# Kernel optimization log

Hardware: AMD Instinct MI355X
Metric: run time of the kernel (lower is better)

Reference implementation:

```python
import jax, jax.numpy as jnp
import numpy as np

DIM, D_INNER, D_STATE, D_CONV, DT_RANK = 768, 1536, 16, 4, 48
B, L = 2, 1024

def setup_inputs() -> dict:
    key = jax.random.key(0)
    ks = jax.random.split(key, 10)
    s = lambda fan: 1.0 / np.sqrt(fan)
    return {
        'x': jax.random.normal(ks[0], (B, L, DIM), jnp.float32),
        'ln_w': jnp.ones((DIM,), jnp.float32),
        'ln_b': jnp.zeros((DIM,), jnp.float32),
        'in_proj_w': jax.random.normal(ks[1], (2 * D_INNER, DIM), jnp.float32) * s(DIM),
        'conv_w': jax.random.normal(ks[2], (D_INNER, D_CONV), jnp.float32) * s(D_CONV),
        'conv_b': jnp.zeros((D_INNER,), jnp.float32),
        'x_proj_w': jax.random.normal(ks[3], (DT_RANK + 2 * D_STATE, D_INNER), jnp.float32) * s(D_INNER),
        'dt_proj_w': jax.random.normal(ks[4], (D_INNER, DT_RANK), jnp.float32) * s(DT_RANK),
        'dt_proj_b': jax.random.normal(ks[5], (D_INNER,), jnp.float32) * 0.1 - 4.0,  # softplus ~ small dt
        'A_log': jnp.log(jnp.broadcast_to(jnp.arange(1, D_STATE + 1, dtype=jnp.float32), (D_INNER, D_STATE))),
        'D_param': jnp.ones((D_INNER,), jnp.float32),
        'out_proj_w': jax.random.normal(ks[6], (DIM, D_INNER), jnp.float32) * s(D_INNER),
    }

def _silu(v):
    return v * jax.nn.sigmoid(v)

def reference(x, ln_w, ln_b, in_proj_w, conv_w, conv_b, x_proj_w,
              dt_proj_w, dt_proj_b, A_log, D_param, out_proj_w):
    Bb, Ll, _ = x.shape
    # LayerNorm (eps=1e-5, torch default)
    mu = jnp.mean(x, -1, keepdims=True)
    var = jnp.mean(jnp.square(x - mu), -1, keepdims=True)
    xn = (x - mu) * jax.lax.rsqrt(var + 1e-5) * ln_w + ln_b
    # in_proj -> (B,L,2*d_inner), split into x-branch and gate z
    xz = xn @ in_proj_w.T
    xm, z = jnp.split(xz, 2, axis=-1)
    # causal depthwise conv1d, kernel D_CONV, left-pad D_CONV-1
    xp = jnp.pad(xm, ((0, 0), (D_CONV - 1, 0), (0, 0)))
    xc = conv_b + sum(xp[:, k:k + Ll, :] * conv_w[:, k] for k in range(D_CONV))
    u = _silu(xc)  # (B,L,d_inner)
    # input-dependent dt, B, C
    dbc = u @ x_proj_w.T
    dt, Bm, Cm = jnp.split(dbc, [DT_RANK, DT_RANK + D_STATE], axis=-1)
    delta = jax.nn.softplus(dt @ dt_proj_w.T + dt_proj_b)  # (B,L,d_inner)
    A = -jnp.exp(A_log)  # (d_inner, d_state), negative
    dA = jnp.exp(delta[..., None] * A)                      # (B,L,D,N)
    dBu = (delta * u)[..., None] * Bm[:, :, None, :]        # (B,L,D,N)
    # linear recurrence h_t = dA_t * h_{t-1} + dBu_t via associative scan
    def comb(e1, e2):
        a1, b1 = e1
        a2, b2 = e2
        return a1 * a2, a2 * b1 + b2
    _, h = jax.lax.associative_scan(comb, (dA, dBu), axis=1)
    y = jnp.einsum('bldn,bln->bld', h, Cm) + u * D_param
    y = y * _silu(z)
    return y @ out_proj_w.T
```

## Files before the change

### kernel.cpp

```cpp
#include <hip/hip_runtime.h>
#include <hip/hip_bf16.h>

#define BATCH 2
#define SEQ   1024
#define DIM   768
#define DI    1536
#define DS    16
#define DCONV 4
#define DTR   48
#define XZW   (2*DI)
#define DBCW  (DTR+2*DS)
#define MROWS (BATCH*SEQ)
#define NCHUNK 32
#define CLEN  (SEQ/NCHUNK)
#define XP_KS 8
#define OP_KS 4

typedef unsigned short ushort_t;
typedef __attribute__((ext_vector_type(8))) short short8;
typedef __attribute__((ext_vector_type(4))) float f32x4;

__device__ __forceinline__ float sigmoidf_(float x) {
    return 1.f / (1.f + __expf(-x));
}

__device__ __forceinline__ ushort_t f2bf(float x) {
    union { float f; unsigned u; } c{x};
    unsigned r = c.u + 0x7FFF + ((c.u >> 16) & 1);
    return (ushort_t)(r >> 16);
}

__device__ __forceinline__ void gload16(const void* g, void* lds) {
    __builtin_amdgcn_global_load_lds(
        (const __attribute__((address_space(1))) void*)g,
        (__attribute__((address_space(3))) void*)lds,
        16, 0, 0);
}

__global__ __launch_bounds__(256) void cvt_bf16(const float* __restrict__ in,
                                                ushort_t* __restrict__ out, int n)
{
    int i = (blockIdx.x * 256 + threadIdx.x) * 8;
    if (i >= n) return;
    float4 a = *(const float4*)(in + i);
    float4 b = *(const float4*)(in + i + 4);
    ushort_t o[8] = { f2bf(a.x), f2bf(a.y), f2bf(a.z), f2bf(a.w),
                      f2bf(b.x), f2bf(b.y), f2bf(b.z), f2bf(b.w) };
    *(ushort4*)(out + i)     = *(ushort4*)o;
    *(ushort4*)(out + i + 4) = *(ushort4*)(o + 4);
}

__global__ __launch_bounds__(256) void at_kernel(const float* __restrict__ A_log,
                                                 float* __restrict__ aT)
{
    int i = blockIdx.x * 256 + threadIdx.x;
    if (i >= DS * DI) return;
    int n = i / DI, d = i % DI;
    aT[i] = -__expf(A_log[d * DS + n]) * 1.44269504f;
}

__global__ __launch_bounds__(256) void reduce_sk4(const float4* __restrict__ part,
                                                  float4* __restrict__ out,
                                                  int count4, int nslices)
{
    int i = blockIdx.x * 256 + threadIdx.x;
    if (i >= count4) return;
    float4 s = part[i];
    for (int z = 1; z < nslices; ++z) {
        float4 p = part[(size_t)z * count4 + i];
        s.x += p.x; s.y += p.y; s.z += p.z; s.w += p.w;
    }
    out[i] = s;
}

__global__ __launch_bounds__(256) void ln_kernel(const float* __restrict__ x,
                                                 const float* __restrict__ w,
                                                 const float* __restrict__ b,
                                                 ushort_t* __restrict__ xn)
{
    __shared__ float part[8];
    int row = blockIdx.x;
    const float* xr = x + (size_t)row * DIM;
    ushort_t* o = xn + (size_t)row * DIM;
    int tid = threadIdx.x;
    int lane = tid & 63, wid = tid >> 6;

    float v0 = xr[tid], v1 = xr[tid + 256], v2 = xr[tid + 512];
    float s = v0 + v1 + v2;
    #pragma unroll
    for (int off = 32; off > 0; off >>= 1) s += __shfl_xor(s, off);
    if (lane == 0) part[wid] = s;
    __syncthreads();
    float mu = (part[0] + part[1] + part[2] + part[3]) * (1.f / DIM);

    float d0 = v0 - mu, d1 = v1 - mu, d2 = v2 - mu;
    float q = d0 * d0 + d1 * d1 + d2 * d2;
    #pragma unroll
    for (int off = 32; off > 0; off >>= 1) q += __shfl_xor(q, off);
    if (lane == 0) part[4 + wid] = q;
    __syncthreads();
    float rstd = rsqrtf((part[4] + part[5] + part[6] + part[7]) * (1.f / DIM) + 1e-5f);

    o[tid]       = f2bf(d0 * rstd * w[tid]       + b[tid]);
    o[tid + 256] = f2bf(d1 * rstd * w[tid + 256] + b[tid + 256]);
    o[tid + 512] = f2bf(d2 * rstd * w[tid + 512] + b[tid + 512]);
}

__global__ __launch_bounds__(256) void gemm_bf16(const ushort_t* __restrict__ A,
                                                 const ushort_t* __restrict__ W,
                                                 float* __restrict__ C,
                                                 int N, int K)
{
    __shared__ __align__(16) ushort_t As[128 * 32];
    __shared__ __align__(16) ushort_t Bs[128 * 32];

    int tid = threadIdx.x;
    int wave = tid >> 6, lane = tid & 63;
    int wr = wave >> 1, wc = wave & 1;
    int l15 = lane & 15, kb = lane >> 4;
    int m0 = blockIdx.y * 128, n0 = blockIdx.x * 128;

    f32x4 acc[4][4] = {};

    for (int k0 = 0; k0 < K; k0 += 32) {
        #pragma unroll
        for (int i = 0; i < 2; ++i) {
            int cbase = i * 256 + wave * 64;
            int c = cbase + lane;
            int row = c >> 2;
            int col = (c & 3) * 8;
            gload16(A + (size_t)(m0 + row) * K + k0 + col, (char*)As + (size_t)cbase * 16);
            gload16(W + (size_t)(n0 + row) * K + k0 + col, (char*)Bs + (size_t)cbase * 16);
        }
        __syncthreads();

        short8 af[4], bfr[4];
        #pragma unroll
        for (int m = 0; m < 4; ++m)
            af[m] = *(const short8*)&As[(wr * 64 + m * 16 + l15) * 32 + kb * 8];
        #pragma unroll
        for (int n = 0; n < 4; ++n)
            bfr[n] = *(const short8*)&Bs[(wc * 64 + n * 16 + l15) * 32 + kb * 8];

        #pragma unroll
        for (int m = 0; m < 4; ++m)
            #pragma unroll
            for (int n = 0; n < 4; ++n)
                acc[m][n] = __builtin_amdgcn_mfma_f32_16x16x32_bf16(af[m], bfr[n], acc[m][n], 0, 0, 0);

        __syncthreads();
    }

    int r0 = m0 + wr * 64 + kb * 4;
    int c0 = n0 + wc * 64 + l15;
    #pragma unroll
    for (int m = 0; m < 4; ++m)
        #pragma unroll
        for (int n = 0; n < 4; ++n) {
            int rr = r0 + m * 16;
            int cc = c0 + n * 16;
            #pragma unroll
            for (int r = 0; r < 4; ++r)
                C[(size_t)(rr + r) * N + cc] = acc[m][n][r];
        }
}

__global__ __launch_bounds__(256) void gemm_bf16_sk(const ushort_t* __restrict__ A,
                                                    const ushort_t* __restrict__ W,
                                                    float* __restrict__ Cpart,
                                                    int N, int Ktot, int Kslice, int M)
{
    __shared__ __align__(16) ushort_t As[128 * 32];
    __shared__ __align__(16) ushort_t Bs[128 * 32];

    int tid = threadIdx.x;
    int wave = tid >> 6, lane = tid & 63;
    int wr = wave >> 1, wc = wave & 1;
    int l15 = lane & 15, kb = lane >> 4;
    int m0 = blockIdx.y * 128, n0 = blockIdx.x * 128;
    int kbase = blockIdx.z * Kslice;
    float* C = Cpart + (size_t)blockIdx.z * M * N;

    f32x4 acc[4][4] = {};

    for (int k0 = kbase; k0 < kbase + Kslice; k0 += 32) {
        #pragma unroll
        for (int i = 0; i < 2; ++i) {
            int cbase = i * 256 + wave * 64;
            int c = cbase + lane;
            int row = c >> 2;
            int col = (c & 3) * 8;
            gload16(A + (size_t)(m0 + row) * Ktot + k0 + col, (char*)As + (size_t)cbase * 16);
            gload16(W + (size_t)(n0 + row) * Ktot + k0 + col, (char*)Bs + (size_t)cbase * 16);
        }
        __syncthreads();

        short8 af[4], bfr[4];
        #pragma unroll
        for (int m = 0; m < 4; ++m)
            af[m] = *(const short8*)&As[(wr * 64 + m * 16 + l15) * 32 + kb * 8];
        #pragma unroll
        for (int n = 0; n < 4; ++n)
            bfr[n] = *(const short8*)&Bs[(wc * 64 + n * 16 + l15) * 32 + kb * 8];

        #pragma unroll
        for (int m = 0; m < 4; ++m)
            #pragma unroll
            for (int n = 0; n < 4; ++n)
                acc[m][n] = __builtin_amdgcn_mfma_f32_16x16x32_bf16(af[m], bfr[n], acc[m][n], 0, 0, 0);

        __syncthreads();
    }

    int r0 = m0 + wr * 64 + kb * 4;
    int c0 = n0 + wc * 64 + l15;
    #pragma unroll
    for (int m = 0; m < 4; ++m)
        #pragma unroll
        for (int n = 0; n < 4; ++n) {
            int rr = r0 + m * 16;
            int cc = c0 + n * 16;
            #pragma unroll
            for (int r = 0; r < 4; ++r)
                C[(size_t)(rr + r) * N + cc] = acc[m][n][r];
        }
}

__global__ __launch_bounds__(256) void gemm_nt(const float* __restrict__ A, int lda,
                                               const float* __restrict__ W, int ldw,
                                               float* __restrict__ C, int ldc,
                                               int N, int K,
                                               const float* __restrict__ bias, int act)
{
    __shared__ float As[64][17];
    __shared__ float Ws[64][17];
    int tid = threadIdx.x;
    int tx = tid & 15;
    int ty = tid >> 4;
    int m0 = blockIdx.y * 64;
    int n0 = blockIdx.x * 64;

    float acc[4][4] = {};

    for (int k0 = 0; k0 < K; k0 += 16) {
        #pragma unroll
        for (int i = 0; i < 4; ++i) {
            int idx = tid + i * 256;
            int r = idx >> 4, c = idx & 15;
            As[r][c] = A[(size_t)(m0 + r) * lda + k0 + c];
            int nr = n0 + r;
            Ws[r][c] = (nr < N) ? W[(size_t)nr * ldw + k0 + c] : 0.f;
        }
        __syncthreads();
        #pragma unroll
        for (int kk = 0; kk < 16; ++kk) {
            float av[4], wv[4];
            #pragma unroll
            for (int i = 0; i < 4; ++i) av[i] = As[ty * 4 + i][kk];
            #pragma unroll
            for (int j = 0; j < 4; ++j) wv[j] = Ws[tx * 4 + j][kk];
            #pragma unroll
            for (int i = 0; i < 4; ++i)
                #pragma unroll
                for (int j = 0; j < 4; ++j)
                    acc[i][j] += av[i] * wv[j];
        }
        __syncthreads();
    }

    #pragma unroll
    for (int i = 0; i < 4; ++i) {
        int m = m0 + ty * 4 + i;
        #pragma unroll
        for (int j = 0; j < 4; ++j) {
            int n = n0 + tx * 4 + j;
            if (n < N) {
                float v = acc[i][j];
                if (bias) v += bias[n];
                if (act == 1) v = (v > 20.f) ? v : log1pf(__expf(v));
                C[(size_t)m * ldc + n] = v;
            }
        }
    }
}

__global__ __launch_bounds__(256) void gemm_nt_sk(const float* __restrict__ A, int lda,
                                                  const float* __restrict__ W, int ldw,
                                                  float* __restrict__ Cpart, int ldc,
                                                  int N, int Kslice, int M)
{
    __shared__ float As[64][17];
    __shared__ float Ws[64][17];
    int tid = threadIdx.x;
    int tx = tid & 15;
    int ty = tid >> 4;
    int m0 = blockIdx.y * 64;
    int n0 = blockIdx.x * 64;
    int kbase = blockIdx.z * Kslice;
    float* C = Cpart + (size_t)blockIdx.z * M * ldc;

    float acc[4][4] = {};

    for (int k0 = kbase; k0 < kbase + Kslice; k0 += 16) {
        #pragma unroll
        for (int i = 0; i < 4; ++i) {
            int idx = tid + i * 256;
            int r = idx >> 4, c = idx & 15;
            As[r][c] = A[(size_t)(m0 + r) * lda + k0 + c];
            int nr = n0 + r;
            Ws[r][c] = (nr < N) ? W[(size_t)nr * ldw + k0 + c] : 0.f;
        }
        __syncthreads();
        #pragma unroll
        for (int kk = 0; kk < 16; ++kk) {
            float av[4], wv[4];
            #pragma unroll
            for (int i = 0; i < 4; ++i) av[i] = As[ty * 4 + i][kk];
            #pragma unroll
            for (int j = 0; j < 4; ++j) wv[j] = Ws[tx * 4 + j][kk];
            #pragma unroll
            for (int i = 0; i < 4; ++i)
                #pragma unroll
                for (int j = 0; j < 4; ++j)
                    acc[i][j] += av[i] * wv[j];
        }
        __syncthreads();
    }

    #pragma unroll
    for (int i = 0; i < 4; ++i) {
        int m = m0 + ty * 4 + i;
        #pragma unroll
        for (int j = 0; j < 4; ++j) {
            int n = n0 + tx * 4 + j;
            if (n < N)
                C[(size_t)m * ldc + n] = acc[i][j];
        }
    }
}

__global__ __launch_bounds__(256) void conv_silu_kernel(const float* __restrict__ xz,
                                                        const float* __restrict__ cw,
                                                        const float* __restrict__ cb,
                                                        float* __restrict__ u)
{
    int idx = blockIdx.x * 256 + threadIdx.x;
    int d4 = idx % (DI / 4);
    int bt = idx / (DI / 4);
    int t = bt % SEQ;
    int b = bt / SEQ;
    int d = d4 * 4;

    float4 w0 = *(const float4*)(cw + (d + 0) * 4);
    float4 w1 = *(const float4*)(cw + (d + 1) * 4);
    float4 w2 = *(const float4*)(cw + (d + 2) * 4);
    float4 w3 = *(const float4*)(cw + (d + 3) * 4);
    const float* wp[4] = { (const float*)&w0, (const float*)&w1,
                           (const float*)&w2, (const float*)&w3 };

    float4 acc = *(const float4*)(cb + d);
    #pragma unroll
    for (int k = 0; k < DCONV; ++k) {
        int tt = t - (DCONV - 1) + k;
        if (tt >= 0) {
            float4 xv = *(const float4*)(xz + (size_t)(b * SEQ + tt) * XZW + d);
            acc.x += xv.x * wp[0][k];
            acc.y += xv.y * wp[1][k];
            acc.z += xv.z * wp[2][k];
            acc.w += xv.w * wp[3][k];
        }
    }
    acc.x *= sigmoidf_(acc.x);
    acc.y *= sigmoidf_(acc.y);
    acc.z *= sigmoidf_(acc.z);
    acc.w *= sigmoidf_(acc.w);
    *(float4*)(u + (size_t)(b * SEQ + t) * DI + d) = acc;
}


__global__ __launch_bounds__(256) void scan_p1(const float* __restrict__ delta,
                                               const float* __restrict__ u,
                                               const float* __restrict__ dbc,
                                               const float* __restrict__ aT,
                                               float* __restrict__ Pw,
                                               float* __restrict__ Sw)
{
    __shared__ float Bs[4][CLEN][DS];
    int tid = threadIdx.x;
    int lane = tid & 63, w = tid >> 6;
    int d = blockIdx.x * 64 + lane;
    int chunk = blockIdx.y * 4 + w;
    int b = blockIdx.z;
    int t0 = chunk * CLEN;

    #pragma unroll
    for (int i = 0; i < 2; ++i) {
        int idx = i * 64 + lane;
        int tl = idx >> 2, c = idx & 3;
        *(float4*)&Bs[w][tl][c * 4] =
            *(const float4*)(dbc + (size_t)(b * SEQ + t0 + tl) * DBCW + DTR + c * 4);
    }

    float a[DS];
    #pragma unroll
    for (int n = 0; n < DS; ++n) a[n] = aT[n * DI + d];

    __syncthreads();

    float P[DS], S[DS];
    #pragma unroll
    for (int n = 0; n < DS; ++n) { P[n] = 1.f; S[n] = 0.f; }

    const float* dp = delta + ((size_t)b * SEQ + t0) * DI + d;
    const float* up = u     + ((size_t)b * SEQ + t0) * DI + d;
    #pragma unroll 4
    for (int j = 0; j < CLEN; ++j) {
        float dlt = dp[(size_t)j * DI];
        float uu  = up[(size_t)j * DI];
        float dltu = dlt * uu;
        #pragma unroll
        for (int n = 0; n < DS; ++n) {
            float dA = exp2f(dlt * a[n]);
            P[n] *= dA;
            S[n] = dA * S[n] + dltu * Bs[w][j][n];
        }
    }

    size_t base = (((size_t)b * NCHUNK + chunk) * DS) * DI + d;
    #pragma unroll
    for (int n = 0; n < DS; ++n) {
        Pw[base + (size_t)n * DI] = P[n];
        Sw[base + (size_t)n * DI] = S[n];
    }
}

__global__ __launch_bounds__(256) void scan_comb(const float* __restrict__ Pw,
                                                 const float* __restrict__ Sw,
                                                 float* __restrict__ Hin)
{
    int d = blockIdx.x * 256 + threadIdx.x;
    int n = blockIdx.y, b = blockIdx.z;
    float h = 0.f;
    for (int c = 0; c < NCHUNK; ++c) {
        size_t idx = (((size_t)b * NCHUNK + c) * DS + n) * DI + d;
        Hin[idx] = h;
        h = Pw[idx] * h + Sw[idx];
    }
}

__global__ __launch_bounds__(256) void scan_p3(const float* __restrict__ delta,
                                               const float* __restrict__ u,
                                               const float* __restrict__ dbc,
                                               const float* __restrict__ xz,
                                               const float* __restrict__ aT,
                                               const float* __restrict__ Dp,
                                               const float* __restrict__ Hin,
                                               ushort_t* __restrict__ y)
{
    __shared__ float Bs[4][CLEN][2 * DS];
    int tid = threadIdx.x;
    int lane = tid & 63, w = tid >> 6;
    int d = blockIdx.x * 64 + lane;
    int chunk = blockIdx.y * 4 + w;
    int b = blockIdx.z;
    int t0 = chunk * CLEN;

    #pragma unroll
    for (int i = 0; i < 4; ++i) {
        int idx = i * 64 + lane;
        int tl = idx >> 3, c = idx & 7;
        *(float4*)&Bs[w][tl][c * 4] =
            *(const float4*)(dbc + (size_t)(b * SEQ + t0 + tl) * DBCW + DTR + c * 4);
    }

    float a[DS], h[DS];
    #pragma unroll
    for (int n = 0; n < DS; ++n) a[n] = aT[n * DI + d];
    size_t hbase = (((size_t)b * NCHUNK + chunk) * DS) * DI + d;
    #pragma unroll
    for (int n = 0; n < DS; ++n) h[n] = Hin[hbase + (size_t)n * DI];

    float Dd = Dp[d];
    __syncthreads();

    const float* dp = delta + ((size_t)b * SEQ + t0) * DI + d;
    const float* up = u     + ((size_t)b * SEQ + t0) * DI + d;
    const float* zp = xz    + ((size_t)b * SEQ + t0) * XZW + DI + d;
    ushort_t* yp    = y     + ((size_t)b * SEQ + t0) * DI + d;

    #pragma unroll 2
    for (int j = 0; j < CLEN; ++j) {
        float dlt = dp[(size_t)j * DI];
        float uu  = up[(size_t)j * DI];
        float dltu = dlt * uu;
        #pragma unroll
        for (int n = 0; n < DS; ++n) {
            float dA = exp2f(dlt * a[n]);
            h[n] = dA * h[n] + dltu * Bs[w][j][n];
        }
        float p0 = 0.f, p1 = 0.f, p2 = 0.f, p3 = 0.f;
        #pragma unroll
        for (int n = 0; n < DS; n += 4) {
            p0 += h[n]     * Bs[w][j][DS + n];
            p1 += h[n + 1] * Bs[w][j][DS + n + 1];
            p2 += h[n + 2] * Bs[w][j][DS + n + 2];
            p3 += h[n + 3] * Bs[w][j][DS + n + 3];
        }
        float p = (p0 + p1) + (p2 + p3);
        float z = zp[(size_t)j * XZW];
        float yv = (p + uu * Dd) * (z * sigmoidf_(z));
        yp[(size_t)j * DI] = f2bf(yv);
    }
}

extern "C" void kernel_launch(void* const* d_in, const int* in_sizes, int n_in,
                              void* d_out, int out_size, void* d_ws, size_t ws_size,
                              hipStream_t stream) {
    const float* x         = (const float*)d_in[0];
    const float* ln_w      = (const float*)d_in[1];
    const float* ln_b      = (const float*)d_in[2];
    const float* in_proj_w = (const float*)d_in[3];
    const float* conv_w    = (const float*)d_in[4];
    const float* conv_b    = (const float*)d_in[5];
    const float* x_proj_w  = (const float*)d_in[6];
    const float* dt_proj_w = (const float*)d_in[7];
    const float* dt_proj_b = (const float*)d_in[8];
    const float* A_log     = (const float*)d_in[9];
    const float* D_param   = (const float*)d_in[10];
    const float* out_proj_w= (const float*)d_in[11];
    float* out = (float*)d_out;

    char* ws = (char*)d_ws;
    size_t off = 0;
    auto alloc = [&](size_t bytes) { void* p = ws + off; off += (bytes + 255) & ~255ull; return p; };

    ushort_t* xn_bf   = (ushort_t*)alloc((size_t)MROWS * DIM * 2);
    ushort_t* w_in_bf = (ushort_t*)alloc((size_t)XZW * DIM * 2);
    ushort_t* w_out_bf= (ushort_t*)alloc((size_t)DIM * DI * 2);
    ushort_t* y_bf    = (ushort_t*)alloc((size_t)MROWS * DI * 2);
    float* xz    = (float*)alloc((size_t)MROWS * XZW * 4);
    float* u     = (float*)alloc((size_t)MROWS * DI * 4);
    float* dbc   = (float*)alloc((size_t)MROWS * DBCW * 4);
    float* delta = (float*)alloc((size_t)MROWS * DI * 4);
    float* aT    = (float*)alloc((size_t)DS * DI * 4);
    float* xpart = (float*)alloc((size_t)XP_KS * MROWS * DBCW * 4);
    float* opart = (float*)alloc((size_t)OP_KS * MROWS * DIM * 4);

    size_t cvol = (size_t)BATCH * NCHUNK * DS * DI;
    float* Pw  = opart;
    float* Sw  = opart + cvol;
    float* Hin = opart + 2 * cvol;

    hipLaunchKernelGGL(cvt_bf16, dim3((XZW * DIM) / 2048), dim3(256), 0, stream,
                       in_proj_w, w_in_bf, XZW * DIM);
    hipLaunchKernelGGL(cvt_bf16, dim3((DIM * DI) / 2048), dim3(256), 0, stream,
                       out_proj_w, w_out_bf, DIM * DI);
    hipLaunchKernelGGL(at_kernel, dim3((DS * DI + 255) / 256), dim3(256), 0, stream,
                       A_log, aT);

    hipLaunchKernelGGL(ln_kernel, dim3(MROWS), dim3(256), 0, stream, x, ln_w, ln_b, xn_bf);

    hipLaunchKernelGGL(gemm_bf16, dim3(XZW / 128, MROWS / 128), dim3(256), 0, stream,
                       xn_bf, w_in_bf, xz, XZW, DIM);

    hipLaunchKernelGGL(conv_silu_kernel, dim3((MROWS * DI / 4) / 256), dim3(256), 0, stream,
                       xz, conv_w, conv_b, u);

    hipLaunchKernelGGL(gemm_nt_sk, dim3((DBCW + 63) / 64, MROWS / 64, XP_KS), dim3(256), 0, stream,
                       u, DI, x_proj_w, DI, xpart, DBCW, DBCW, DI / XP_KS, MROWS);
    hipLaunchKernelGGL(reduce_sk4, dim3((MROWS * DBCW / 4 + 255) / 256), dim3(256), 0, stream,
                       (const float4*)xpart, (float4*)dbc, MROWS * DBCW / 4, XP_KS);

    hipLaunchKernelGGL(gemm_nt, dim3(DI / 64, MROWS / 64), dim3(256), 0, stream,
                       dbc, DBCW, dt_proj_w, DTR, delta, DI, DI, DTR, dt_proj_b, 1);

    hipLaunchKernelGGL(scan_p1, dim3(DI / 64, NCHUNK / 4, BATCH), dim3(256), 0, stream,
                       delta, u, dbc, aT, Pw, Sw);
    hipLaunchKernelGGL(scan_comb, dim3(DI / 256, DS, BATCH), dim3(256), 0, stream,
                       Pw, Sw, Hin);
    hipLaunchKernelGGL(scan_p3, dim3(DI / 64, NCHUNK / 4, BATCH), dim3(256), 0, stream,
                       delta, u, dbc, xz, aT, D_param, Hin, y_bf);

    hipLaunchKernelGGL(gemm_bf16_sk, dim3(DIM / 128, MROWS / 128, OP_KS), dim3(256), 0, stream,
                       y_bf, w_out_bf, opart, DIM, DI, DI / OP_KS, MROWS);
    hipLaunchKernelGGL(reduce_sk4, dim3((MROWS * DIM / 4 + 255) / 256), dim3(256), 0, stream,
                       (const float4*)opart, (float4*)out, MROWS * DIM / 4, OP_KS);
}
```

Measured before the change: 205.7 us.

## Move x_proj and dt_proj GEMMs to bf16 MFMA with padded weights

Replaces the scalar fp32 split-K x_proj GEMM and the dt_proj GEMM with bf16 MFMA kernels. The conv kernel now also writes a bf16 copy of u, x_proj_w is padded to 128 rows, and dt_proj_w is padded to K=64. A new reduce step emits both the fp32 dbc and a padded bf16 dt tile. The aim is to cut the cost of the slow scalar SIMT GEMMs, at the price of lower precision in dt, B and C and some extra writes and padded work.

```diff
diff --git a/kernel.cpp b/kernel.cpp
--- a/kernel.cpp
+++ b/kernel.cpp
@@ -15,6 +15,7 @@
 #define CLEN  (SEQ/NCHUNK)
 #define XP_KS 8
 #define OP_KS 4
+#define XPN   128
 
 typedef unsigned short ushort_t;
 typedef __attribute__((ext_vector_type(8))) short short8;
@@ -50,13 +51,29 @@
     *(ushort4*)(out + i + 4) = *(ushort4*)(o + 4);
 }
 
-__global__ __launch_bounds__(256) void at_kernel(const float* __restrict__ A_log,
-                                                 float* __restrict__ aT)
+__global__ __launch_bounds__(256) void prep_small(const float* __restrict__ A_log,
+                                                  const float* __restrict__ x_proj_w,
+                                                  const float* __restrict__ dt_proj_w,
+                                                  float* __restrict__ aT,
+                                                  ushort_t* __restrict__ xpw_pad,
+                                                  ushort_t* __restrict__ dtw_bf)
 {
     int i = blockIdx.x * 256 + threadIdx.x;
-    if (i >= DS * DI) return;
-    int n = i / DI, d = i % DI;
-    aT[i] = -__expf(A_log[d * DS + n]) * 1.44269504f;
+    const int NA = DS * DI;
+    const int NX = XPN * DI;
+    const int NDT = DI * 64;
+    if (i < NA) {
+        int n = i / DI, d = i % DI;
+        aT[i] = -__expf(A_log[d * DS + n]) * 1.44269504f;
+    } else if (i < NA + NX) {
+        int j = i - NA;
+        int r = j / DI, c = j % DI;
+        xpw_pad[j] = (r < DBCW) ? f2bf(x_proj_w[r * DI + c]) : (ushort_t)0;
+    } else if (i < NA + NX + NDT) {
+        int j = i - NA - NX;
+        int r = j / 64, c = j % 64;
+        dtw_bf[j] = (c < DTR) ? f2bf(dt_proj_w[r * DTR + c]) : (ushort_t)0;
+    }
 }
 
 __global__ __launch_bounds__(256) void reduce_sk4(const float4* __restrict__ part,
@@ -71,6 +88,21 @@
         s.x += p.x; s.y += p.y; s.z += p.z; s.w += p.w;
     }
     out[i] = s;
+}
+
+__global__ __launch_bounds__(256) void reduce_dbc(const float* __restrict__ part,
+                                                  float* __restrict__ dbc,
+                                                  ushort_t* __restrict__ dtb)
+{
+    int i = blockIdx.x * 256 + threadIdx.x;
+    if (i >= MROWS * XPN) return;
+    float s = 0.f;
+    #pragma unroll
+    for (int z = 0; z < XP_KS; ++z)
+        s += part[(size_t)z * MROWS * XPN + i];
+    int r = i / XPN, c = i % XPN;
+    if (c < DBCW) dbc[(size_t)r * DBCW + c] = s;
+    if (c < 64)   dtb[(size_t)r * 64 + c] = (c < DTR) ? f2bf(s) : (ushort_t)0;
 }
 
 __global__ __launch_bounds__(256) void ln_kernel(const float* __restrict__ x,
@@ -226,123 +258,75 @@
         }
 }
 
-__global__ __launch_bounds__(256) void gemm_nt(const float* __restrict__ A, int lda,
-                                               const float* __restrict__ W, int ldw,
-                                               float* __restrict__ C, int ldc,
-                                               int N, int K,
-                                               const float* __restrict__ bias, int act)
-{
-    __shared__ float As[64][17];
-    __shared__ float Ws[64][17];
+__global__ __launch_bounds__(256) void gemm_dt(const ushort_t* __restrict__ A,
+                                               const ushort_t* __restrict__ W,
+                                               const float* __restrict__ bias,
+                                               float* __restrict__ C)
+{
+    __shared__ __align__(16) ushort_t As[128 * 32];
+    __shared__ __align__(16) ushort_t Bs[128 * 32];
+
     int tid = threadIdx.x;
-    int tx = tid & 15;
-    int ty = tid >> 4;
-    int m0 = blockIdx.y * 64;
-    int n0 = blockIdx.x * 64;
-
-    float acc[4][4] = {};
-
-    for (int k0 = 0; k0 < K; k0 += 16) {
-        #pragma unroll
-        for (int i = 0; i < 4; ++i) {
-            int idx = tid + i * 256;
-            int r = idx >> 4, c = idx & 15;
-            As[r][c] = A[(size_t)(m0 + r) * lda + k0 + c];
-            int nr = n0 + r;
-            Ws[r][c] = (nr < N) ? W[(size_t)nr * ldw + k0 + c] : 0.f;
+    int wave = tid >> 6, lane = tid & 63;
+    int wr = wave >> 1, wc = wave & 1;
+    int l15 = lane & 15, kb = lane >> 4;
+    int m0 = blockIdx.y * 128, n0 = blockIdx.x * 128;
+
+    f32x4 acc[4][4] = {};
+
+    #pragma unroll
+    for (int k0 = 0; k0 < 64; k0 += 32) {
+        #pragma unroll
+        for (int i = 0; i < 2; ++i) {
+            int cbase = i * 256 + wave * 64;
+            int c = cbase + lane;
+            int row = c >> 2;
+            int col = (c & 3) * 8;
+            gload16(A + (size_t)(m0 + row) * 64 + k0 + col, (char*)As + (size_t)cbase * 16);
+            gload16(W + (size_t)(n0 + row) * 64 + k0 + col, (char*)Bs + (size_t)cbase * 16);
         }
         __syncthreads();
-        #pragma unroll
-        for (int kk = 0; kk < 16; ++kk) {
-            float av[4], wv[4];
+
+        short8 af[4], bfr[4];
+        #pragma unroll
+        for (int m = 0; m < 4; ++m)
+            af[m] = *(const short8*)&As[(wr * 64 + m * 16 + l15) * 32 + kb * 8];
+        #pragma unroll
+        for (int n = 0; n < 4; ++n)
+            bfr[n] = *(const short8*)&Bs[(wc * 64 + n * 16 + l15) * 32 + kb * 8];
+
+        #pragma unroll
+        for (int m = 0; m < 4; ++m)
             #pragma unroll
-            for (int i = 0; i < 4; ++i) av[i] = As[ty * 4 + i][kk];
+            for (int n = 0; n < 4; ++n)
+                acc[m][n] = __builtin_amdgcn_mfma_f32_16x16x32_bf16(af[m], bfr[n], acc[m][n], 0, 0, 0);
+
+        __syncthreads();
+    }
+
+    int r0 = m0 + wr * 64 + kb * 4;
+    int c0 = n0 + wc * 64 + l15;
+    #pragma unroll
+    for (int m = 0; m < 4; ++m)
+        #pragma unroll
+        for (int n = 0; n < 4; ++n) {
+            int rr = r0 + m * 16;
+            int cc = c0 + n * 16;
+            float bv = bias[cc];
             #pragma unroll
-            for (int j = 0; j < 4; ++j) wv[j] = Ws[tx * 4 + j][kk];
-            #pragma unroll
-            for (int i = 0; i < 4; ++i)
-                #pragma unroll
-                for (int j = 0; j < 4; ++j)
-                    acc[i][j] += av[i] * wv[j];
-        }
-        __syncthreads();
-    }
-
-    #pragma unroll
-    for (int i = 0; i < 4; ++i) {
-        int m = m0 + ty * 4 + i;
-        #pragma unroll
-        for (int j = 0; j < 4; ++j) {
-            int n = n0 + tx * 4 + j;
-            if (n < N) {
-                float v = acc[i][j];
-                if (bias) v += bias[n];
-                if (act == 1) v = (v > 20.f) ? v : log1pf(__expf(v));
-                C[(size_t)m * ldc + n] = v;
+            for (int r = 0; r < 4; ++r) {
+                float v = acc[m][n][r] + bv;
+                v = (v > 20.f) ? v : log1pf(__expf(v));
+                C[(size_t)(rr + r) * DI + cc] = v;
             }
         }
-    }
-}
-
-__global__ __launch_bounds__(256) void gemm_nt_sk(const float* __restrict__ A, int lda,
-                                                  const float* __restrict__ W, int ldw,
-                                                  float* __restrict__ Cpart, int ldc,
-                                                  int N, int Kslice, int M)
-{
-    __shared__ float As[64][17];
-    __shared__ float Ws[64][17];
-    int tid = threadIdx.x;
-    int tx = tid & 15;
-    int ty = tid >> 4;
-    int m0 = blockIdx.y * 64;
-    int n0 = blockIdx.x * 64;
-    int kbase = blockIdx.z * Kslice;
-    float* C = Cpart + (size_t)blockIdx.z * M * ldc;
-
-    float acc[4][4] = {};
-
-    for (int k0 = kbase; k0 < kbase + Kslice; k0 += 16) {
-        #pragma unroll
-        for (int i = 0; i < 4; ++i) {
-            int idx = tid + i * 256;
-            int r = idx >> 4, c = idx & 15;
-            As[r][c] = A[(size_t)(m0 + r) * lda + k0 + c];
-            int nr = n0 + r;
-            Ws[r][c] = (nr < N) ? W[(size_t)nr * ldw + k0 + c] : 0.f;
-        }
-        __syncthreads();
-        #pragma unroll
-        for (int kk = 0; kk < 16; ++kk) {
-            float av[4], wv[4];
-            #pragma unroll
-            for (int i = 0; i < 4; ++i) av[i] = As[ty * 4 + i][kk];
-            #pragma unroll
-            for (int j = 0; j < 4; ++j) wv[j] = Ws[tx * 4 + j][kk];
-            #pragma unroll
-            for (int i = 0; i < 4; ++i)
-                #pragma unroll
-                for (int j = 0; j < 4; ++j)
-                    acc[i][j] += av[i] * wv[j];
-        }
-        __syncthreads();
-    }
-
-    #pragma unroll
-    for (int i = 0; i < 4; ++i) {
-        int m = m0 + ty * 4 + i;
-        #pragma unroll
-        for (int j = 0; j < 4; ++j) {
-            int n = n0 + tx * 4 + j;
-            if (n < N)
-                C[(size_t)m * ldc + n] = acc[i][j];
-        }
-    }
 }
 
 __global__ __launch_bounds__(256) void conv_silu_kernel(const float* __restrict__ xz,
                                                         const float* __restrict__ cw,
                                                         const float* __restrict__ cb,
-                                                        float* __restrict__ u)
+                                                        float* __restrict__ u,
+                                                        ushort_t* __restrict__ u_bf)
 {
     int idx = blockIdx.x * 256 + threadIdx.x;
     int d4 = idx % (DI / 4);
@@ -374,9 +358,11 @@
     acc.y *= sigmoidf_(acc.y);
     acc.z *= sigmoidf_(acc.z);
     acc.w *= sigmoidf_(acc.w);
-    *(float4*)(u + (size_t)(b * SEQ + t) * DI + d) = acc;
-}
-
+    size_t o = (size_t)(b * SEQ + t) * DI + d;
+    *(float4*)(u + o) = acc;
+    ushort4 ob = { f2bf(acc.x), f2bf(acc.y), f2bf(acc.z), f2bf(acc.w) };
+    *(ushort4*)(u_bf + o) = ob;
+}
 
 __global__ __launch_bounds__(256) void scan_p1(const float* __restrict__ delta,
                                                const float* __restrict__ u,
@@ -538,12 +524,16 @@
     ushort_t* w_in_bf = (ushort_t*)alloc((size_t)XZW * DIM * 2);
     ushort_t* w_out_bf= (ushort_t*)alloc((size_t)DIM * DI * 2);
     ushort_t* y_bf    = (ushort_t*)alloc((size_t)MROWS * DI * 2);
+    ushort_t* u_bf    = (ushort_t*)alloc((size_t)MROWS * DI * 2);
+    ushort_t* xpw_pad = (ushort_t*)alloc((size_t)XPN * DI * 2);
+    ushort_t* dtw_bf  = (ushort_t*)alloc((size_t)DI * 64 * 2);
+    ushort_t* dtb     = (ushort_t*)alloc((size_t)MROWS * 64 * 2);
     float* xz    = (float*)alloc((size_t)MROWS * XZW * 4);
     float* u     = (float*)alloc((size_t)MROWS * DI * 4);
     float* dbc   = (float*)alloc((size_t)MROWS * DBCW * 4);
     float* delta = (float*)alloc((size_t)MROWS * DI * 4);
     float* aT    = (float*)alloc((size_t)DS * DI * 4);
-    float* xpart = (float*)alloc((size_t)XP_KS * MROWS * DBCW * 4);
+    float* xpart = (float*)alloc((size_t)XP_KS * MROWS * XPN * 4);
     float* opart = (float*)alloc((size_t)OP_KS * MROWS * DIM * 4);
 
     size_t cvol = (size_t)BATCH * NCHUNK * DS * DI;
@@ -555,8 +545,9 @@
                        in_proj_w, w_in_bf, XZW * DIM);
     hipLaunchKernelGGL(cvt_bf16, dim3((DIM * DI) / 2048), dim3(256), 0, stream,
                        out_proj_w, w_out_bf, DIM * DI);
-    hipLaunchKernelGGL(at_kernel, dim3((DS * DI + 255) / 256), dim3(256), 0, stream,
-                       A_log, aT);
+    hipLaunchKernelGGL(prep_small,
+                       dim3((DS * DI + XPN * DI + DI * 64 + 255) / 256), dim3(256), 0, stream,
+                       A_log, x_proj_w, dt_proj_w, aT, xpw_pad, dtw_bf);
 
     hipLaunchKernelGGL(ln_kernel, dim3(MROWS), dim3(256), 0, stream, x, ln_w, ln_b, xn_bf);
 
@@ -564,15 +555,15 @@
                        xn_bf, w_in_bf, xz, XZW, DIM);
 
     hipLaunchKernelGGL(conv_silu_kernel, dim3((MROWS * DI / 4) / 256), dim3(256), 0, stream,
-                       xz, conv_w, conv_b, u);
-
-    hipLaunchKernelGGL(gemm_nt_sk, dim3((DBCW + 63) / 64, MROWS / 64, XP_KS), dim3(256), 0, stream,
-                       u, DI, x_proj_w, DI, xpart, DBCW, DBCW, DI / XP_KS, MROWS);
-    hipLaunchKernelGGL(reduce_sk4, dim3((MROWS * DBCW / 4 + 255) / 256), dim3(256), 0, stream,
-                       (const float4*)xpart, (float4*)dbc, MROWS * DBCW / 4, XP_KS);
-
-    hipLaunchKernelGGL(gemm_nt, dim3(DI / 64, MROWS / 64), dim3(256), 0, stream,
-                       dbc, DBCW, dt_proj_w, DTR, delta, DI, DI, DTR, dt_proj_b, 1);
+                       xz, conv_w, conv_b, u, u_bf);
+
+    hipLaunchKernelGGL(gemm_bf16_sk, dim3(XPN / 128, MROWS / 128, XP_KS), dim3(256), 0, stream,
+                       u_bf, xpw_pad, xpart, XPN, DI, DI / XP_KS, MROWS);
+    hipLaunchKernelGGL(reduce_dbc, dim3((MROWS * XPN + 255) / 256), dim3(256), 0, stream,
+                       xpart, dbc, dtb);
+
+    hipLaunchKernelGGL(gemm_dt, dim3(DI / 128, MROWS / 128), dim3(256), 0, stream,
+                       dtb, dtw_bf, dt_proj_b, delta);
 
     hipLaunchKernelGGL(scan_p1, dim3(DI / 64, NCHUNK / 4, BATCH), dim3(256), 0, stream,
                        delta, u, dbc, aT, Pw, Sw);
```

Result: faster. 184.7 us (-10.2%).
